# Optimization experiments

Hardware: AMD Instinct MI355X
Metric: run time of the kernel (lower is better)

Reference implementation:

```python
import jax, jax.numpy as jnp
import numpy as np

# Module hyperparameters (see init_kwargs)
P1, P2 = 32, 32      # num_patches_h, num_patches_w (256/8)
H1, W2 = 8, 8        # patch_size
CH = 3               # input channels
CI, SI = 768, 4      # num_cores, rfs_per_capsule (capsule_size=256, rf_size=64)
KOUT, LOUT = 256, 4  # output_cores, slots per output core
PROBA = 0.1          # connection_proba


def setup_inputs() -> dict:
    key = jax.random.key(0)
    kx, kc = jax.random.split(key)
    x = jax.random.normal(kx, (128, 256, 256, 3), dtype=jnp.float32)
    # fast_scrramble: fixed random-sparse binary connectivity tensor
    # [source_core, source_slot, dest_core, dest_slot]
    C = jax.random.bernoulli(kc, PROBA, (CI, SI, KOUT, LOUT)).astype(jnp.float32)
    return {"x": x, "C": C}


def reference(x, C):
    b = x.shape[0]
    # 'b (p1 h1) (p2 w2) c -> b p1 p2 h1 w2 c'
    x = x.reshape(b, P1, H1, P2, W2, CH).transpose(0, 1, 3, 2, 4, 5)
    # 'b p1 p2 h1 w2 c -> b h1 w2 (p1 p2 c)'
    x = x.transpose(0, 3, 4, 1, 2, 5).reshape(b, H1, W2, P1 * P2 * CH)
    # 'b h1 w2 (ci si) -> b ci si h1 w2'
    x = x.reshape(b, H1, W2, CI, SI).transpose(0, 3, 4, 1, 2)
    # Literal einsum from the source: no shared labels between operands,
    # so this is sum_{c,s} x (per b,h,w) times sum_{i,j} C (per k,l).
    return jnp.einsum('bcshw,ijkl->bklhw', x, C)
```

## Files before the change

kernel.cpp:

```cpp
#include <hip/hip_runtime.h>


__global__ __launch_bounds__(192) void reduce_partials(
    const float4* __restrict__ x4,
    const float4* __restrict__ C4,
    float*  __restrict__ cpart,
    float*  __restrict__ xpart)
{
    const int t   = threadIdx.x;
    const int blk = blockIdx.x;

    if (blk < 96) {
        const size_t r0 = (size_t)blk * 32;
        for (int c4 = t; c4 < 256; c4 += 192) {
            const float4* p = C4 + r0 * 256 + c4;
            float ax = 0, ay = 0, az = 0, aw = 0;
            float bx = 0, by = 0, bz = 0, bw = 0;
#pragma unroll
            for (int r = 0; r < 32; r += 2) {
                float4 v0 = p[0];
                float4 v1 = p[256];
                ax += v0.x; ay += v0.y; az += v0.z; aw += v0.w;
                bx += v1.x; by += v1.y; bz += v1.z; bw += v1.w;
                p += 512;
            }
            float4 s;
            s.x = ax + bx; s.y = ay + by; s.z = az + bz; s.w = aw + bw;
            ((float4*)cpart)[blk * 256 + c4] = s;
        }
        return;
    }

    const int xb    = blk - 96;
    const int b     = xb >> 3;
    const int chunk = xb & 7;
    const float4* base = x4 + ((size_t)b * 256 + (size_t)chunk * 32) * 192 + t;

    float4 acc[8];
#pragma unroll
    for (int h = 0; h < 8; ++h) { acc[h].x = acc[h].y = acc[h].z = acc[h].w = 0.f; }

#pragma unroll
    for (int h = 0; h < 8; ++h) {
#pragma unroll
        for (int j = 0; j < 4; ++j) {
            float4 v = base[(size_t)(h + 8 * j) * 192];
            acc[h].x += v.x; acc[h].y += v.y; acc[h].z += v.z; acc[h].w += v.w;
        }
    }

    __shared__ float4 ldsv[192][9];
    __shared__ float  plane[8][193];
#pragma unroll
    for (int h = 0; h < 8; ++h) ldsv[t][h] = acc[h];
    __syncthreads();

    {
        const int h2  = t / 48;
        const int tau = t - h2 * 48;
#pragma unroll
        for (int k = 0; k < 2; ++k) {
            const int hh = h2 + 4 * k;
            float4 s0 = ldsv[tau      ][hh];
            float4 s1 = ldsv[tau +  48][hh];
            float4 s2 = ldsv[tau +  96][hh];
            float4 s3 = ldsv[tau + 144][hh];
            plane[hh][4 * tau + 0] = s0.x + s1.x + s2.x + s3.x;
            plane[hh][4 * tau + 1] = s0.y + s1.y + s2.y + s3.y;
            plane[hh][4 * tau + 2] = s0.z + s1.z + s2.z + s3.z;
            plane[hh][4 * tau + 3] = s0.w + s1.w + s2.w + s3.w;
        }
    }
    __syncthreads();

    if (t < 64) {
        const int h = t >> 3, w = t & 7;
        float s = 0.f;
#pragma unroll
        for (int g = 0; g < 8; ++g) {
            const float* pp = &plane[h][24 * g + 3 * w];
            s += pp[0] + pp[1] + pp[2];
        }
        xpart[xb * 64 + t] = s;
    }
}

__global__ __launch_bounds__(256) void finalize_sums(
    const float* __restrict__ xpart,
    const float* __restrict__ cpart,
    float* __restrict__ sxf,
    float* __restrict__ scf)
{
    const int blk = blockIdx.x;
    const int t   = threadIdx.x;
    if (blk < 32) {
        const int tid = blk * 256 + t;
        const float* p = xpart + (size_t)(tid >> 6) * 8 * 64 + (tid & 63);
        float s = 0.f;
#pragma unroll
        for (int j = 0; j < 8; ++j) s += p[j * 64];
        sxf[tid] = s;
    } else {
        const int col = (blk - 32) * 256 + t;
        float s = 0.f;
#pragma unroll 8
        for (int g = 0; g < 96; ++g) s += cpart[g * 1024 + col];
        scf[col] = s;
    }
}

__global__ __launch_bounds__(256) void expand_out(
    const float* __restrict__ sxf,
    const float* __restrict__ scf,
    float4* __restrict__ out4)
{
    const int t   = threadIdx.x;
    const int klc = blockIdx.x;
    const int b   = blockIdx.y;

    __shared__ float4 sxv[16];
    __shared__ float  scl[128];

    if (t < 16) {
        sxv[t] = ((const float4*)(sxf + b * 64))[t];
    } else if (t >= 64 && t < 192) {
        scl[t - 64] = scf[klc * 128 + (t - 64)];
    }
    __syncthreads();

    float4* ob = out4 + (size_t)b * 16384 + (size_t)klc * 2048;
#pragma unroll
    for (int k = 0; k < 8; ++k) {
        const int idx = k * 256 + t;
        const float4 v = sxv[idx & 15];
        const float  s = scl[idx >> 4];
        float4 r;
        r.x = v.x * s; r.y = v.y * s; r.z = v.z * s; r.w = v.w * s;
        ob[idx] = r;
    }
}

extern "C" void kernel_launch(void* const* d_in, const int* in_sizes, int n_in,
                              void* d_out, int out_size, void* d_ws, size_t ws_size,
                              hipStream_t stream) {
    const float4* x4 = (const float4*)d_in[0];
    const float4* C4 = (const float4*)d_in[1];

    float* cpart = (float*)d_ws;
    float* xpart = cpart + 96 * 1024;
    float* sxf   = xpart + 1024 * 64;
    float* scf   = sxf + 128 * 64;

    reduce_partials<<<dim3(96 + 1024), 192, 0, stream>>>(x4, C4, cpart, xpart);
    finalize_sums<<<dim3(36),          256, 0, stream>>>(xpart, cpart, sxf, scf);
    expand_out<<<dim3(8, 128),         256, 0, stream>>>(sxf, scf, (float4*)d_out);
}
```

Baseline: 173.2 us.

## Move LDS cross-thread reduction from streaming kernel into finalize kernel

The streaming reduction kernel no longer uses shared memory or barriers. Each thread dumps its eight per-row float4 accumulators to a workspace buffer. The finalize kernel, now with one block per batch, re-reads the eight chunks, sums them, and performs the LDS transpose and channel reduction. This is meant to raise occupancy and shorten the bandwidth-bound kernel, at the cost of roughly 25MB of extra global writes and reads plus a larger workspace.

Result: slower. 179.2 us (+3.4%).

```diff
diff --git a/kernel.cpp b/kernel.cpp
--- a/kernel.cpp
+++ b/kernel.cpp
@@ -5,7 +5,7 @@
     const float4* __restrict__ x4,
     const float4* __restrict__ C4,
     float*  __restrict__ cpart,
-    float*  __restrict__ xpart)
+    float4* __restrict__ xdump)
 {
     const int t   = threadIdx.x;
     const int blk = blockIdx.x;
@@ -49,13 +49,50 @@
         }
     }
 
+    float4* dst = xdump + (size_t)xb * 8 * 192 + t;
+#pragma unroll
+    for (int h = 0; h < 8; ++h) dst[h * 192] = acc[h];
+}
+
+__global__ __launch_bounds__(256) void finalize_sums(
+    const float4* __restrict__ xdump,
+    const float*  __restrict__ cpart,
+    float* __restrict__ sxf,
+    float* __restrict__ scf)
+{
+    const int blk = blockIdx.x;
+    const int t   = threadIdx.x;
+
+    if (blk >= 128) {
+        const int col = (blk - 128) * 256 + t;
+        float s = 0.f;
+#pragma unroll 8
+        for (int g = 0; g < 96; ++g) s += cpart[g * 1024 + col];
+        scf[col] = s;
+        return;
+    }
+
     __shared__ float4 ldsv[192][9];
     __shared__ float  plane[8][193];
+
+    if (t < 192) {
+        float4 acc[8];
 #pragma unroll
-    for (int h = 0; h < 8; ++h) ldsv[t][h] = acc[h];
+        for (int h = 0; h < 8; ++h) { acc[h].x = acc[h].y = acc[h].z = acc[h].w = 0.f; }
+        const float4* src = xdump + (size_t)blk * 8 * 8 * 192 + t;
+#pragma unroll
+        for (int s = 0; s < 8; ++s)
+#pragma unroll
+            for (int h = 0; h < 8; ++h) {
+                float4 v = src[(size_t)(s * 8 + h) * 192];
+                acc[h].x += v.x; acc[h].y += v.y; acc[h].z += v.z; acc[h].w += v.w;
+            }
+#pragma unroll
+        for (int h = 0; h < 8; ++h) ldsv[t][h] = acc[h];
+    }
     __syncthreads();
 
-    {
+    if (t < 192) {
         const int h2  = t / 48;
         const int tau = t - h2 * 48;
 #pragma unroll
@@ -81,31 +118,7 @@
             const float* pp = &plane[h][24 * g + 3 * w];
             s += pp[0] + pp[1] + pp[2];
         }
-        xpart[xb * 64 + t] = s;
-    }
-}
-
-__global__ __launch_bounds__(256) void finalize_sums(
-    const float* __restrict__ xpart,
-    const float* __restrict__ cpart,
-    float* __restrict__ sxf,
-    float* __restrict__ scf)
-{
-    const int blk = blockIdx.x;
-    const int t   = threadIdx.x;
-    if (blk < 32) {
-        const int tid = blk * 256 + t;
-        const float* p = xpart + (size_t)(tid >> 6) * 8 * 64 + (tid & 63);
-        float s = 0.f;
-#pragma unroll
-        for (int j = 0; j < 8; ++j) s += p[j * 64];
-        sxf[tid] = s;
-    } else {
-        const int col = (blk - 32) * 256 + t;
-        float s = 0.f;
-#pragma unroll 8
-        for (int g = 0; g < 96; ++g) s += cpart[g * 1024 + col];
-        scf[col] = s;
+        sxf[blk * 64 + t] = s;
     }
 }
 
@@ -146,12 +159,12 @@
     const float4* x4 = (const float4*)d_in[0];
     const float4* C4 = (const float4*)d_in[1];
 
-    float* cpart = (float*)d_ws;
-    float* xpart = cpart + 96 * 1024;
-    float* sxf   = xpart + 1024 * 64;
-    float* scf   = sxf + 128 * 64;
+    float*  cpart = (float*)d_ws;
+    float4* xdump = (float4*)(cpart + 96 * 1024);
+    float*  sxf   = (float*)(xdump + (size_t)1024 * 8 * 192);
+    float*  scf   = sxf + 128 * 64;
 
-    reduce_partials<<<dim3(96 + 1024), 192, 0, stream>>>(x4, C4, cpart, xpart);
-    finalize_sums<<<dim3(36),          256, 0, stream>>>(xpart, cpart, sxf, scf);
+    reduce_partials<<<dim3(96 + 1024), 192, 0, stream>>>(x4, C4, cpart, xdump);
+    finalize_sums<<<dim3(132),         256, 0, stream>>>(xdump, cpart, sxf, scf);
     expand_out<<<dim3(8, 128),         256, 0, stream>>>(sxf, scf, (float4*)d_out);
 }
```

## Assign one x block per (batch,h) row to finish x sums in-kernel

Applied to the files above, without the earlier changes.

Each x-reduction block now owns one (batch, h) pair and strides over all 32 patch rows, so it writes final per-(b,h,w) sums directly and no second pass over x partials is needed. The finalize kernel shrinks to a C-only column collapse. x loads use nontemporal hints, the output stores are nontemporal, and the C blocks move to the end of the grid. The per-thread accumulator shrinks from eight float4 to one, but each block now does fewer loads with a long dependent add chain, which could reduce memory-level parallelism.

New measurement: 167.1 us, median of 2. -3.5%, faster.

```diff
diff --git a/kernel.cpp b/kernel.cpp
--- a/kernel.cpp
+++ b/kernel.cpp
@@ -1,17 +1,20 @@
 #include <hip/hip_runtime.h>
 
 
-__global__ __launch_bounds__(192) void reduce_partials(
+typedef float nf4 __attribute__((ext_vector_type(4)));
+
+__global__ __launch_bounds__(192, 3) void reduce_partials(
     const float4* __restrict__ x4,
     const float4* __restrict__ C4,
     float*  __restrict__ cpart,
-    float*  __restrict__ xpart)
+    float*  __restrict__ sxf)
 {
     const int t   = threadIdx.x;
     const int blk = blockIdx.x;
 
-    if (blk < 96) {
-        const size_t r0 = (size_t)blk * 32;
+    if (blk >= 1024) {
+        const int cb = blk - 1024;
+        const size_t r0 = (size_t)cb * 32;
         for (int c4 = t; c4 < 256; c4 += 192) {
             const float4* p = C4 + r0 * 256 + c4;
             float ax = 0, ay = 0, az = 0, aw = 0;
@@ -26,82 +29,65 @@
             }
             float4 s;
             s.x = ax + bx; s.y = ay + by; s.z = az + bz; s.w = aw + bw;
-            ((float4*)cpart)[blk * 256 + c4] = s;
+            ((float4*)cpart)[cb * 256 + c4] = s;
         }
         return;
     }
 
-    const int xb    = blk - 96;
-    const int b     = xb >> 3;
-    const int chunk = xb & 7;
-    const float4* base = x4 + ((size_t)b * 256 + (size_t)chunk * 32) * 192 + t;
+    const int b = blk >> 3;
+    const int h = blk & 7;
+    const nf4* base = (const nf4*)(x4 + ((size_t)b * 256 + h) * 192 + t);
 
-    float4 acc[8];
+    nf4 acc = (nf4)(0.f);
 #pragma unroll
-    for (int h = 0; h < 8; ++h) { acc[h].x = acc[h].y = acc[h].z = acc[h].w = 0.f; }
-
-#pragma unroll
-    for (int h = 0; h < 8; ++h) {
-#pragma unroll
-        for (int j = 0; j < 4; ++j) {
-            float4 v = base[(size_t)(h + 8 * j) * 192];
-            acc[h].x += v.x; acc[h].y += v.y; acc[h].z += v.z; acc[h].w += v.w;
-        }
+    for (int j = 0; j < 32; ++j) {
+        nf4 v = __builtin_nontemporal_load(&base[(size_t)j * 8 * 192]);
+        acc += v;
     }
 
-    __shared__ float4 ldsv[192][9];
-    __shared__ float  plane[8][193];
-#pragma unroll
-    for (int h = 0; h < 8; ++h) ldsv[t][h] = acc[h];
+    __shared__ float4 arr[192];
+    __shared__ float4 arr2[48];
+    __shared__ float  cls[24];
+
+    arr[t].x = acc.x; arr[t].y = acc.y; arr[t].z = acc.z; arr[t].w = acc.w;
     __syncthreads();
 
-    {
-        const int h2  = t / 48;
-        const int tau = t - h2 * 48;
-#pragma unroll
-        for (int k = 0; k < 2; ++k) {
-            const int hh = h2 + 4 * k;
-            float4 s0 = ldsv[tau      ][hh];
-            float4 s1 = ldsv[tau +  48][hh];
-            float4 s2 = ldsv[tau +  96][hh];
-            float4 s3 = ldsv[tau + 144][hh];
-            plane[hh][4 * tau + 0] = s0.x + s1.x + s2.x + s3.x;
-            plane[hh][4 * tau + 1] = s0.y + s1.y + s2.y + s3.y;
-            plane[hh][4 * tau + 2] = s0.z + s1.z + s2.z + s3.z;
-            plane[hh][4 * tau + 3] = s0.w + s1.w + s2.w + s3.w;
-        }
+    if (t < 48) {
+        float4 a0 = arr[t], a1 = arr[t + 48], a2 = arr[t + 96], a3 = arr[t + 144];
+        float4 s;
+        s.x = a0.x + a1.x + a2.x + a3.x;
+        s.y = a0.y + a1.y + a2.y + a3.y;
+        s.z = a0.z + a1.z + a2.z + a3.z;
+        s.w = a0.w + a1.w + a2.w + a3.w;
+        arr2[t] = s;
     }
     __syncthreads();
 
-    if (t < 64) {
-        const int h = t >> 3, w = t & 7;
-        float s = 0.f;
+    if (t < 6) {
+        float4 s; s.x = s.y = s.z = s.w = 0.f;
 #pragma unroll
         for (int g = 0; g < 8; ++g) {
-            const float* pp = &plane[h][24 * g + 3 * w];
-            s += pp[0] + pp[1] + pp[2];
+            float4 v = arr2[t + 6 * g];
+            s.x += v.x; s.y += v.y; s.z += v.z; s.w += v.w;
         }
-        xpart[xb * 64 + t] = s;
+        cls[4 * t + 0] = s.x;
+        cls[4 * t + 1] = s.y;
+        cls[4 * t + 2] = s.z;
+        cls[4 * t + 3] = s.w;
+    }
+    __syncthreads();
+
+    if (t < 8) {
+        sxf[b * 64 + h * 8 + t] = cls[3 * t] + cls[3 * t + 1] + cls[3 * t + 2];
     }
 }
 
-__global__ __launch_bounds__(256) void finalize_sums(
-    const float* __restrict__ xpart,
+__global__ __launch_bounds__(192) void collapse_C(
     const float* __restrict__ cpart,
-    float* __restrict__ sxf,
     float* __restrict__ scf)
 {
-    const int blk = blockIdx.x;
-    const int t   = threadIdx.x;
-    if (blk < 32) {
-        const int tid = blk * 256 + t;
-        const float* p = xpart + (size_t)(tid >> 6) * 8 * 64 + (tid & 63);
-        float s = 0.f;
-#pragma unroll
-        for (int j = 0; j < 8; ++j) s += p[j * 64];
-        sxf[tid] = s;
-    } else {
-        const int col = (blk - 32) * 256 + t;
+    const int col = blockIdx.x * 192 + threadIdx.x;
+    if (col < 1024) {
         float s = 0.f;
 #pragma unroll 8
         for (int g = 0; g < 96; ++g) s += cpart[g * 1024 + col];
@@ -134,9 +120,9 @@
         const int idx = k * 256 + t;
         const float4 v = sxv[idx & 15];
         const float  s = scl[idx >> 4];
-        float4 r;
+        nf4 r;
         r.x = v.x * s; r.y = v.y * s; r.z = v.z * s; r.w = v.w * s;
-        ob[idx] = r;
+        __builtin_nontemporal_store(r, (nf4*)&ob[idx]);
     }
 }
 
@@ -147,11 +133,10 @@
     const float4* C4 = (const float4*)d_in[1];
 
     float* cpart = (float*)d_ws;
-    float* xpart = cpart + 96 * 1024;
-    float* sxf   = xpart + 1024 * 64;
+    float* sxf   = cpart + 96 * 1024;
     float* scf   = sxf + 128 * 64;
 
-    reduce_partials<<<dim3(96 + 1024), 192, 0, stream>>>(x4, C4, cpart, xpart);
-    finalize_sums<<<dim3(36),          256, 0, stream>>>(xpart, cpart, sxf, scf);
+    reduce_partials<<<dim3(1024 + 96), 192, 0, stream>>>(x4, C4, cpart, sxf);
+    collapse_C<<<dim3(6),              192, 0, stream>>>(cpart, scf);
     expand_out<<<dim3(8, 128),         256, 0, stream>>>(sxf, scf, (float4*)d_out);
 }
```
